# Performance work log

Measured on AMD Instinct MI355X. Metric: run time of the kernel, lower is better.

Reference implementation:

```python
import jax, jax.numpy as jnp
import numpy as np

N_NODES = 100000
N_EDGES = 1600000
D = 64


def setup_inputs() -> dict:
    key = jax.random.key(0)
    k1, k2, k3 = jax.random.split(key, 3)
    x = jax.random.normal(k1, (N_NODES, D), dtype=jnp.float32)
    edge_index = jax.random.randint(k2, (2, N_EDGES), 0, N_NODES, dtype=jnp.int32)
    W = jax.random.normal(k3, (D, D), dtype=jnp.float32) * 0.05  # linear weight [out_dim, in_dim]
    b = jnp.zeros((D,), dtype=jnp.float32)
    return {"x": x, "edge_index": edge_index, "W": W, "b": b}


def reference(x, edge_index, W, b):
    n = x.shape[0]
    # add self loops
    loops = jnp.arange(n, dtype=edge_index.dtype)
    src = jnp.concatenate([edge_index[0], loops])
    dst = jnp.concatenate([edge_index[1], loops])
    # in-degree (counting self loops) via scatter-add of ones onto dst
    deg = jax.ops.segment_sum(jnp.ones_like(src, dtype=x.dtype), dst, num_segments=n)
    deg_inv_sqrt = jnp.where(deg > 0, jax.lax.rsqrt(jnp.maximum(deg, 1.0)) * (deg > 0), 0.0)
    deg_inv_sqrt = jnp.where(deg > 0, deg ** -0.5, 0.0)
    # per-edge symmetric normalization, gather-scale-scatter
    norm = deg_inv_sqrt[src] * deg_inv_sqrt[dst]  # [E+N]
    msgs = x[src] * norm[:, None]                  # [E+N, D] big irregular gather
    out = jax.ops.segment_sum(msgs, dst, num_segments=n)  # scatter-add to nodes
    # dense linear
    return out @ W.T + b
```

## Files before the change

### kernel.cpp

```cpp
#include <hip/hip_runtime.h>


#define BSHIFT 7
#define BNODES 128
#define CAP 3072
#define EPB 4096
#define SMEM_BYTES 32768

__device__ inline unsigned short f2b_rn(float f) {
    unsigned u = __float_as_uint(f);
    unsigned r = u + 0x7FFFu + ((u >> 16) & 1u);
    return (unsigned short)(r >> 16);
}
__device__ inline float b2f(unsigned short h) {
    return __uint_as_float(((unsigned)h) << 16);
}

__global__ __launch_bounds__(256) void fused_gemm_scatter_kernel(
    const float* __restrict__ x, const float* __restrict__ W,
    float4* __restrict__ yf,
    const int* __restrict__ ei, int* __restrict__ gcur,
    unsigned int* __restrict__ grec,
    int n, int e, int nbuck, int sblocks) {
    __shared__ __align__(16) unsigned char smem[SMEM_BYTES];
    int t = threadIdx.x;

    if ((int)blockIdx.x < sblocks) {
        unsigned int* lrec = (unsigned int*)smem;
        unsigned short* lbk = (unsigned short*)(smem + 16384);
        int* lh = (int*)(smem + 24576);
        int* lbase = lh + nbuck;
        for (int i = t; i < nbuck; i += 256) lh[i] = 0;
        __syncthreads();
        int e0 = blockIdx.x * EPB;
        int m = e - e0;
        if (m > EPB) m = EPB;
        for (int i = t; i < m; i += 256) {
            int g = e0 + i;
            int s = ei[g];
            int d = ei[e + g];
            int b = d >> BSHIFT;
            lrec[i] = ((unsigned int)s << BSHIFT) | (unsigned int)(d & (BNODES - 1));
            lbk[i] = (unsigned short)b;
            atomicAdd(&lh[b], 1);
        }
        __syncthreads();
        for (int b = t; b < nbuck; b += 256) {
            int c = lh[b];
            lbase[b] = c ? atomicAdd(&gcur[b], c) : 0;
            lh[b] = 0;
        }
        __syncthreads();
        for (int i = t; i < m; i += 256) {
            int b = lbk[i];
            int pos = lbase[b] + atomicAdd(&lh[b], 1);
            if (pos < CAP)
                grec[(size_t)b * CAP + pos] = lrec[i];
        }
    } else {
        float4* At4 = (float4*)smem;
        float4* Wt4 = (float4*)(smem + 16384);
        int m0 = ((int)blockIdx.x - sblocks) * 64;

#pragma unroll
        for (int j = 0; j < 4; ++j) {
            int idx = t + j * 256;
            int k = idx & 63;
            int r = idx >> 6;
            float4 wv;
            wv.x = W[(size_t)(4 * r + 0) * 64 + k];
            wv.y = W[(size_t)(4 * r + 1) * 64 + k];
            wv.z = W[(size_t)(4 * r + 2) * 64 + k];
            wv.w = W[(size_t)(4 * r + 3) * 64 + k];
            Wt4[k * 16 + (r ^ (k & 15))] = wv;
            float4 av;
            int gm = m0 + 4 * r;
            av.x = (gm + 0 < n) ? x[(size_t)(gm + 0) * 64 + k] : 0.f;
            av.y = (gm + 1 < n) ? x[(size_t)(gm + 1) * 64 + k] : 0.f;
            av.z = (gm + 2 < n) ? x[(size_t)(gm + 2) * 64 + k] : 0.f;
            av.w = (gm + 3 < n) ? x[(size_t)(gm + 3) * 64 + k] : 0.f;
            At4[k * 16 + (r ^ (k & 15))] = av;
        }
        __syncthreads();

        int tx = t & 15, ty = t >> 4;
        float acc[4][4];
#pragma unroll
        for (int i = 0; i < 4; ++i)
#pragma unroll
            for (int j = 0; j < 4; ++j) acc[i][j] = 0.f;

#pragma unroll 8
        for (int k = 0; k < 64; ++k) {
            float4 a = At4[k * 16 + (ty ^ (k & 15))];
            float4 w = Wt4[k * 16 + (tx ^ (k & 15))];
            float av[4] = {a.x, a.y, a.z, a.w};
            float wv[4] = {w.x, w.y, w.z, w.w};
#pragma unroll
            for (int i = 0; i < 4; ++i)
#pragma unroll
                for (int j = 0; j < 4; ++j) acc[i][j] += av[i] * wv[j];
        }

#pragma unroll
        for (int i = 0; i < 4; ++i) {
            int gm = m0 + ty * 4 + i;
            if (gm < n) {
                float4 v;
                v.x = acc[i][0]; v.y = acc[i][1];
                v.z = acc[i][2]; v.w = acc[i][3];
                yf[(size_t)gm * 16 + tx] = v;
            }
        }
    }
}

__global__ __launch_bounds__(256) void bucket_scale_kernel(
    const unsigned int* __restrict__ grec, const int* __restrict__ gcur,
    const float4* __restrict__ yf, ushort4* __restrict__ yh, int n) {
    __shared__ int lh[BNODES];
    int t = threadIdx.x;
    int b = blockIdx.x;
    size_t base = (size_t)b * CAP;
    int cnt = gcur[b];
    if (cnt > CAP) cnt = CAP;
    int node0 = b << BSHIFT;
    if (t < BNODES) lh[t] = 0;
    __syncthreads();
    for (int i = t; i < cnt; i += 256)
        atomicAdd(&lh[grec[base + i] & (BNODES - 1)], 1);
    __syncthreads();
#pragma unroll
    for (int j = 0; j < 8; ++j) {
        int idx = t + j * 256;
        int nd = idx >> 4, fq = idx & 15;
        int node = node0 + nd;
        if (node < n) {
            float dn = rsqrtf((float)(lh[nd] + 1));
            float4 v = yf[(size_t)node * 16 + fq];
            ushort4 h;
            h.x = f2b_rn(v.x * dn);
            h.y = f2b_rn(v.y * dn);
            h.z = f2b_rn(v.z * dn);
            h.w = f2b_rn(v.w * dn);
            yh[(size_t)node * 16 + fq] = h;
        }
    }
}

__global__ __launch_bounds__(512, 4) void csr_gather_kernel(
    const unsigned int* __restrict__ grec, const int* __restrict__ gcur,
    const ushort4* __restrict__ yh, const float* __restrict__ bias,
    float4* __restrict__ out, int n) {
    __shared__ unsigned int sorted[CAP];
    __shared__ int lh[BNODES];
    __shared__ int ls[BNODES + 1];
    __shared__ int wtot;
    int t = threadIdx.x;
    int b = blockIdx.x;
    size_t base = (size_t)b * CAP;
    int cnt = gcur[b];
    if (cnt > CAP) cnt = CAP;
    int node0 = b << BSHIFT;

    if (t < BNODES) lh[t] = 0;
    __syncthreads();
    for (int i = t; i < cnt; i += 512)
        atomicAdd(&lh[grec[base + i] & (BNODES - 1)], 1);
    __syncthreads();
    int c = 0, ex = 0;
    if (t < BNODES) {
        c = lh[t];
        int lane64 = t & 63;
        int v = c;
#pragma unroll
        for (int o = 1; o < 64; o <<= 1) {
            int u = __shfl_up(v, o, 64);
            if (lane64 >= o) v += u;
        }
        if (t == 63) wtot = v;
        ex = v - c;
    }
    __syncthreads();
    if (t >= 64 && t < BNODES) ex += wtot;
    if (t < BNODES) {
        ls[t] = ex;
        lh[t] = 0;
        if (t == BNODES - 1) ls[BNODES] = ex + c;
    }
    __syncthreads();
    for (int i = t; i < cnt; i += 512) {
        unsigned int r = grec[base + i];
        int nd = r & (BNODES - 1);
        int pos = ls[nd] + atomicAdd(&lh[nd], 1);
        sorted[pos] = r >> BSHIFT;
    }
    __syncthreads();

    int wave = t >> 6;
    int lane = t & 63;
    int grp = lane >> 4;
    int fq = lane & 15;
    float4 bb = ((const float4*)bias)[fq];
    for (int i = 0; i < 16; ++i) {
        int nd = wave * 16 + i;
        int node = node0 + nd;
        if (node >= n) break;
        int beg = ls[nd];
        int end = ls[nd + 1];
        float dn = rsqrtf((float)(end - beg) + 1.0f);
        float4 acc = {0.f, 0.f, 0.f, 0.f};
        if (grp == 0) {
            ushort4 h = yh[(size_t)node * 16 + fq];
            acc.x = b2f(h.x); acc.y = b2f(h.y);
            acc.z = b2f(h.z); acc.w = b2f(h.w);
        }
        int j = beg + grp;
        for (; j + 12 < end; j += 16) {
            int s0 = (int)sorted[j];
            int s1 = (int)sorted[j + 4];
            int s2 = (int)sorted[j + 8];
            int s3 = (int)sorted[j + 12];
            ushort4 h0 = yh[(size_t)s0 * 16 + fq];
            ushort4 h1 = yh[(size_t)s1 * 16 + fq];
            ushort4 h2 = yh[(size_t)s2 * 16 + fq];
            ushort4 h3 = yh[(size_t)s3 * 16 + fq];
            acc.x += b2f(h0.x) + b2f(h1.x) + b2f(h2.x) + b2f(h3.x);
            acc.y += b2f(h0.y) + b2f(h1.y) + b2f(h2.y) + b2f(h3.y);
            acc.z += b2f(h0.z) + b2f(h1.z) + b2f(h2.z) + b2f(h3.z);
            acc.w += b2f(h0.w) + b2f(h1.w) + b2f(h2.w) + b2f(h3.w);
        }
        for (; j < end; j += 4) {
            int s = (int)sorted[j];
            ushort4 h = yh[(size_t)s * 16 + fq];
            acc.x += b2f(h.x); acc.y += b2f(h.y);
            acc.z += b2f(h.z); acc.w += b2f(h.w);
        }
        for (int m = 16; m < 64; m <<= 1) {
            acc.x += __shfl_xor(acc.x, m);
            acc.y += __shfl_xor(acc.y, m);
            acc.z += __shfl_xor(acc.z, m);
            acc.w += __shfl_xor(acc.w, m);
        }
        if (lane < 16) {
            float4 o;
            o.x = acc.x * dn + bb.x;
            o.y = acc.y * dn + bb.y;
            o.z = acc.z * dn + bb.z;
            o.w = acc.w * dn + bb.w;
            out[(size_t)node * 16 + lane] = o;
        }
    }
}

extern "C" void kernel_launch(void* const* d_in, const int* in_sizes, int n_in,
                              void* d_out, int out_size, void* d_ws, size_t ws_size,
                              hipStream_t stream) {
    const float* x    = (const float*)d_in[0];
    const int*   ei   = (const int*)d_in[1];
    const float* W    = (const float*)d_in[2];
    const float* bias = (const float*)d_in[3];
    float* out = (float*)d_out;

    int n = in_sizes[0] / 64;
    int e = in_sizes[1] / 2;
    int nbuck = (n + BNODES - 1) / BNODES;

    auto align = [](size_t v) { return (v + 255) & ~(size_t)255; };
    char* p = (char*)d_ws;
    int* gcur = (int*)p;          p += align((size_t)nbuck * 4);
    unsigned int* grec = (unsigned int*)p;  p += align((size_t)nbuck * CAP * 4);
    float4* yf = (float4*)p;      p += align((size_t)n * 64 * 4);
    ushort4* yh = (ushort4*)p;

    int sblocks = (e + EPB - 1) / EPB;
    int gblocks = (n + 63) / 64;

    hipMemsetAsync(gcur, 0, (size_t)nbuck * 4, stream);
    fused_gemm_scatter_kernel<<<sblocks + gblocks, 256, 0, stream>>>(
        x, W, yf, ei, gcur, grec, n, e, nbuck, sblocks);
    bucket_scale_kernel<<<nbuck, 256, 0, stream>>>(grec, gcur, yf, yh, n);
    csr_gather_kernel<<<nbuck, 512, 0, stream>>>(grec, gcur, yh, bias,
                                                 (float4*)out, n);
}
```

Baseline: 167.1 us.

## Compute degrees with global atomics and fuse scaling into GEMM epilogue

Adds a separate degree kernel that counts destination occurrences with global atomics. The GEMM blocks then scale their outputs by rsqrt(deg+1) and write bf16 directly, so the fp32 intermediate buffer and the bucket_scale kernel are removed. This trades a full fp32 write and read of the node features for 1.6M global atomic increments in an extra launch, plus a larger memset.

```diff
diff --git a/kernel.cpp b/kernel.cpp
--- a/kernel.cpp
+++ b/kernel.cpp
@@ -16,9 +16,26 @@
     return __uint_as_float(((unsigned)h) << 16);
 }
 
+__global__ __launch_bounds__(256) void deg_kernel(
+    const int* __restrict__ dst, int* __restrict__ deg, int e) {
+    int t = blockIdx.x * blockDim.x + threadIdx.x;
+    int stride = gridDim.x * blockDim.x;
+    int e4 = e >> 2;
+    const int4* d4 = (const int4*)dst;
+    for (int i = t; i < e4; i += stride) {
+        int4 v = d4[i];
+        atomicAdd(&deg[v.x], 1);
+        atomicAdd(&deg[v.y], 1);
+        atomicAdd(&deg[v.z], 1);
+        atomicAdd(&deg[v.w], 1);
+    }
+    for (int i = (e4 << 2) + t; i < e; i += stride)
+        atomicAdd(&deg[dst[i]], 1);
+}
+
 __global__ __launch_bounds__(256) void fused_gemm_scatter_kernel(
     const float* __restrict__ x, const float* __restrict__ W,
-    float4* __restrict__ yf,
+    ushort4* __restrict__ yh, const int* __restrict__ deg,
     const int* __restrict__ ei, int* __restrict__ gcur,
     unsigned int* __restrict__ grec,
     int n, int e, int nbuck, int sblocks) {
@@ -106,44 +123,14 @@
         for (int i = 0; i < 4; ++i) {
             int gm = m0 + ty * 4 + i;
             if (gm < n) {
-                float4 v;
-                v.x = acc[i][0]; v.y = acc[i][1];
-                v.z = acc[i][2]; v.w = acc[i][3];
-                yf[(size_t)gm * 16 + tx] = v;
+                float dn = rsqrtf((float)(deg[gm] + 1));
+                ushort4 h;
+                h.x = f2b_rn(acc[i][0] * dn);
+                h.y = f2b_rn(acc[i][1] * dn);
+                h.z = f2b_rn(acc[i][2] * dn);
+                h.w = f2b_rn(acc[i][3] * dn);
+                yh[(size_t)gm * 16 + tx] = h;
             }
-        }
-    }
-}
-
-__global__ __launch_bounds__(256) void bucket_scale_kernel(
-    const unsigned int* __restrict__ grec, const int* __restrict__ gcur,
-    const float4* __restrict__ yf, ushort4* __restrict__ yh, int n) {
-    __shared__ int lh[BNODES];
-    int t = threadIdx.x;
-    int b = blockIdx.x;
-    size_t base = (size_t)b * CAP;
-    int cnt = gcur[b];
-    if (cnt > CAP) cnt = CAP;
-    int node0 = b << BSHIFT;
-    if (t < BNODES) lh[t] = 0;
-    __syncthreads();
-    for (int i = t; i < cnt; i += 256)
-        atomicAdd(&lh[grec[base + i] & (BNODES - 1)], 1);
-    __syncthreads();
-#pragma unroll
-    for (int j = 0; j < 8; ++j) {
-        int idx = t + j * 256;
-        int nd = idx >> 4, fq = idx & 15;
-        int node = node0 + nd;
-        if (node < n) {
-            float dn = rsqrtf((float)(lh[nd] + 1));
-            float4 v = yf[(size_t)node * 16 + fq];
-            ushort4 h;
-            h.x = f2b_rn(v.x * dn);
-            h.y = f2b_rn(v.y * dn);
-            h.z = f2b_rn(v.z * dn);
-            h.w = f2b_rn(v.w * dn);
-            yh[(size_t)node * 16 + fq] = h;
         }
     }
 }
@@ -269,17 +256,17 @@
     auto align = [](size_t v) { return (v + 255) & ~(size_t)255; };
     char* p = (char*)d_ws;
     int* gcur = (int*)p;          p += align((size_t)nbuck * 4);
+    int* deg = (int*)p;           p += align((size_t)n * 4);
     unsigned int* grec = (unsigned int*)p;  p += align((size_t)nbuck * CAP * 4);
-    float4* yf = (float4*)p;      p += align((size_t)n * 64 * 4);
     ushort4* yh = (ushort4*)p;
 
     int sblocks = (e + EPB - 1) / EPB;
     int gblocks = (n + 63) / 64;
 
-    hipMemsetAsync(gcur, 0, (size_t)nbuck * 4, stream);
+    hipMemsetAsync(gcur, 0, (char*)grec - (char*)gcur, stream);
+    deg_kernel<<<1024, 256, 0, stream>>>(ei + e, deg, e);
     fused_gemm_scatter_kernel<<<sblocks + gblocks, 256, 0, stream>>>(
-        x, W, yf, ei, gcur, grec, n, e, nbuck, sblocks);
-    bucket_scale_kernel<<<nbuck, 256, 0, stream>>>(grec, gcur, yf, yh, n);
+        x, W, yh, deg, ei, gcur, grec, n, e, nbuck, sblocks);
     csr_gather_kernel<<<nbuck, 512, 0, stream>>>(grec, gcur, yh, bias,
                                                  (float4*)out, n);
 }
```

After: 222.9 us. +33.4%, slower.

## Write bf16 GEMM output directly and apply source degree scaling in gather

Applied to the files above, without the earlier changes.

The GEMM stage now writes bf16 values straight to the half-precision buffer instead of an fp32 intermediate. The middle kernel only computes a per-node inverse-sqrt degree array, so the fp32 read and bf16 rewrite pass over all node features disappears. In exchange, the gather loop issues an extra scattered 4-byte load of dnorm per edge and does a multiply per element. Values are also rounded to bf16 before scaling rather than after, which changes rounding slightly.

```diff
diff --git a/kernel.cpp b/kernel.cpp
--- a/kernel.cpp
+++ b/kernel.cpp
@@ -18,7 +18,7 @@
 
 __global__ __launch_bounds__(256) void fused_gemm_scatter_kernel(
     const float* __restrict__ x, const float* __restrict__ W,
-    float4* __restrict__ yf,
+    ushort4* __restrict__ yh,
     const int* __restrict__ ei, int* __restrict__ gcur,
     unsigned int* __restrict__ grec,
     int n, int e, int nbuck, int sblocks) {
@@ -106,51 +106,41 @@
         for (int i = 0; i < 4; ++i) {
             int gm = m0 + ty * 4 + i;
             if (gm < n) {
-                float4 v;
-                v.x = acc[i][0]; v.y = acc[i][1];
-                v.z = acc[i][2]; v.w = acc[i][3];
-                yf[(size_t)gm * 16 + tx] = v;
+                ushort4 h;
+                h.x = f2b_rn(acc[i][0]);
+                h.y = f2b_rn(acc[i][1]);
+                h.z = f2b_rn(acc[i][2]);
+                h.w = f2b_rn(acc[i][3]);
+                yh[(size_t)gm * 16 + tx] = h;
             }
         }
     }
 }
 
-__global__ __launch_bounds__(256) void bucket_scale_kernel(
+__global__ __launch_bounds__(256) void dnorm_kernel(
     const unsigned int* __restrict__ grec, const int* __restrict__ gcur,
-    const float4* __restrict__ yf, ushort4* __restrict__ yh, int n) {
+    float* __restrict__ dnorm, int n) {
     __shared__ int lh[BNODES];
     int t = threadIdx.x;
     int b = blockIdx.x;
     size_t base = (size_t)b * CAP;
     int cnt = gcur[b];
     if (cnt > CAP) cnt = CAP;
-    int node0 = b << BSHIFT;
     if (t < BNODES) lh[t] = 0;
     __syncthreads();
     for (int i = t; i < cnt; i += 256)
         atomicAdd(&lh[grec[base + i] & (BNODES - 1)], 1);
     __syncthreads();
-#pragma unroll
-    for (int j = 0; j < 8; ++j) {
-        int idx = t + j * 256;
-        int nd = idx >> 4, fq = idx & 15;
-        int node = node0 + nd;
-        if (node < n) {
-            float dn = rsqrtf((float)(lh[nd] + 1));
-            float4 v = yf[(size_t)node * 16 + fq];
-            ushort4 h;
-            h.x = f2b_rn(v.x * dn);
-            h.y = f2b_rn(v.y * dn);
-            h.z = f2b_rn(v.z * dn);
-            h.w = f2b_rn(v.w * dn);
-            yh[(size_t)node * 16 + fq] = h;
-        }
+    if (t < BNODES) {
+        int node = (b << BSHIFT) + t;
+        if (node < n) dnorm[node] = rsqrtf((float)lh[t] + 1.0f);
     }
 }
 
 __global__ __launch_bounds__(512, 4) void csr_gather_kernel(
     const unsigned int* __restrict__ grec, const int* __restrict__ gcur,
-    const ushort4* __restrict__ yh, const float* __restrict__ bias,
+    const ushort4* __restrict__ yh, const float* __restrict__ dnorm,
+    const float* __restrict__ bias,
     float4* __restrict__ out, int n) {
     __shared__ unsigned int sorted[CAP];
     __shared__ int lh[BNODES];
@@ -212,8 +202,8 @@
         float4 acc = {0.f, 0.f, 0.f, 0.f};
         if (grp == 0) {
             ushort4 h = yh[(size_t)node * 16 + fq];
-            acc.x = b2f(h.x); acc.y = b2f(h.y);
-            acc.z = b2f(h.z); acc.w = b2f(h.w);
+            acc.x = dn * b2f(h.x); acc.y = dn * b2f(h.y);
+            acc.z = dn * b2f(h.z); acc.w = dn * b2f(h.w);
         }
         int j = beg + grp;
         for (; j + 12 < end; j += 16) {
@@ -225,16 +215,25 @@
             ushort4 h1 = yh[(size_t)s1 * 16 + fq];
             ushort4 h2 = yh[(size_t)s2 * 16 + fq];
             ushort4 h3 = yh[(size_t)s3 * 16 + fq];
-            acc.x += b2f(h0.x) + b2f(h1.x) + b2f(h2.x) + b2f(h3.x);
-            acc.y += b2f(h0.y) + b2f(h1.y) + b2f(h2.y) + b2f(h3.y);
-            acc.z += b2f(h0.z) + b2f(h1.z) + b2f(h2.z) + b2f(h3.z);
-            acc.w += b2f(h0.w) + b2f(h1.w) + b2f(h2.w) + b2f(h3.w);
+            float d0 = dnorm[s0];
+            float d1 = dnorm[s1];
+            float d2 = dnorm[s2];
+            float d3 = dnorm[s3];
+            acc.x += d0 * b2f(h0.x); acc.x += d1 * b2f(h1.x);
+            acc.x += d2 * b2f(h2.x); acc.x += d3 * b2f(h3.x);
+            acc.y += d0 * b2f(h0.y); acc.y += d1 * b2f(h1.y);
+            acc.y += d2 * b2f(h2.y); acc.y += d3 * b2f(h3.y);
+            acc.z += d0 * b2f(h0.z); acc.z += d1 * b2f(h1.z);
+            acc.z += d2 * b2f(h2.z); acc.z += d3 * b2f(h3.z);
+            acc.w += d0 * b2f(h0.w); acc.w += d1 * b2f(h1.w);
+            acc.w += d2 * b2f(h2.w); acc.w += d3 * b2f(h3.w);
         }
         for (; j < end; j += 4) {
             int s = (int)sorted[j];
             ushort4 h = yh[(size_t)s * 16 + fq];
-            acc.x += b2f(h.x); acc.y += b2f(h.y);
-            acc.z += b2f(h.z); acc.w += b2f(h.w);
+            float d0 = dnorm[s];
+            acc.x += d0 * b2f(h.x); acc.y += d0 * b2f(h.y);
+            acc.z += d0 * b2f(h.z); acc.w += d0 * b2f(h.w);
         }
         for (int m = 16; m < 64; m <<= 1) {
             acc.x += __shfl_xor(acc.x, m);
@@ -268,9 +267,9 @@
 
     auto align = [](size_t v) { return (v + 255) & ~(size_t)255; };
     char* p = (char*)d_ws;
-    int* gcur = (int*)p;          p += align((size_t)nbuck * 4);
+    int* gcur = (int*)p;                    p += align((size_t)nbuck * 4);
     unsigned int* grec = (unsigned int*)p;  p += align((size_t)nbuck * CAP * 4);
-    float4* yf = (float4*)p;      p += align((size_t)n * 64 * 4);
+    float* dnorm = (float*)p;               p += align((size_t)n * 4);
     ushort4* yh = (ushort4*)p;
 
     int sblocks = (e + EPB - 1) / EPB;
@@ -278,8 +277,8 @@
 
     hipMemsetAsync(gcur, 0, (size_t)nbuck * 4, stream);
     fused_gemm_scatter_kernel<<<sblocks + gblocks, 256, 0, stream>>>(
-        x, W, yf, ei, gcur, grec, n, e, nbuck, sblocks);
-    bucket_scale_kernel<<<nbuck, 256, 0, stream>>>(grec, gcur, yf, yh, n);
-    csr_gather_kernel<<<nbuck, 512, 0, stream>>>(grec, gcur, yh, bias,
+        x, W, yh, ei, gcur, grec, n, e, nbuck, sblocks);
+    dnorm_kernel<<<nbuck, 256, 0, stream>>>(grec, gcur, dnorm, n);
+    csr_gather_kernel<<<nbuck, 512, 0, stream>>>(grec, gcur, yh, dnorm, bias,
                                                  (float4*)out, n);
 }
```

Result: no change. 165.9 us (-0.7%).
